# Optimization experiments

Hardware: AMD Instinct MI355X
Metric: run time of the kernel (lower is better)

Reference implementation:

```python
import jax, jax.numpy as jnp
import numpy as np

N_NODES = 100000
IN_DIM = 64
HID = 64
N_EDGES = 1600000
EPS = 1e-5
SLOPE = 0.01  # F.leaky_relu default


def _glorot(key, shape):
    fan_in, fan_out = shape[1], shape[0]
    lim = jnp.sqrt(6.0 / (fan_in + fan_out))
    return jax.random.uniform(key, shape, jnp.float32, -lim, lim)


def setup_inputs() -> dict:
    key = jax.random.key(0)
    ks = jax.random.split(key, 8)
    x = jax.random.normal(ks[0], (N_NODES, IN_DIM), jnp.float32)
    src = jax.random.randint(ks[1], (N_EDGES,), 0, N_NODES, jnp.int32)
    dst = jax.random.randint(ks[2], (N_EDGES,), 0, N_NODES, jnp.int32)
    edge_index = jnp.stack([src, dst])  # [2, E]
    return {
        "x": x,
        "edge_index": edge_index,
        "W_self1": _glorot(ks[3], (HID, IN_DIM)),
        "W_neigh1": _glorot(ks[4], (HID, IN_DIM)),
        "b1": jnp.zeros((HID,), jnp.float32),
        "gamma1": jnp.ones((HID,), jnp.float32),
        "beta1": jnp.zeros((HID,), jnp.float32),
        "W_self2": _glorot(ks[5], (HID, HID)),
        "W_neigh2": _glorot(ks[6], (HID, HID)),
        "b2": jnp.zeros((HID,), jnp.float32),
        "gamma2": jnp.ones((HID,), jnp.float32),
        "beta2": jnp.zeros((HID,), jnp.float32),
    }


def _sage_mean(h, src, dst, W_self, W_neigh, b):
    # neighbor mean aggregation: mean of src features at each dst node
    msg_sum = jax.ops.segment_sum(h[src], dst, num_segments=N_NODES)  # [N, d]
    deg = jax.ops.segment_sum(jnp.ones_like(dst, jnp.float32), dst, num_segments=N_NODES)
    h_neigh = msg_sum / jnp.maximum(deg, 1.0)[:, None]  # isolated nodes -> 0
    return h @ W_self.T + h_neigh @ W_neigh.T + b


def _bn(h, gamma, beta):
    mu = jnp.mean(h, axis=0)
    var = jnp.mean(jnp.square(h - mu), axis=0)
    return (h - mu) * jax.lax.rsqrt(var + EPS) * gamma + beta


def reference(x, edge_index, W_self1, W_neigh1, b1, gamma1, beta1,
              W_self2, W_neigh2, b2, gamma2, beta2):
    src, dst = edge_index[0], edge_index[1]
    h = _sage_mean(x, src, dst, W_self1, W_neigh1, b1)
    h = jax.nn.leaky_relu(_bn(h, gamma1, beta1), SLOPE)
    h = _sage_mean(h, src, dst, W_self2, W_neigh2, b2)
    h = jax.nn.leaky_relu(_bn(h, gamma2, beta2), SLOPE)
    return h
```

## Files before the change

kernel.cpp:

```cpp
#include <hip/hip_runtime.h>

#define EPS 1e-5f
#define SLOPE 0.01f

typedef short bf16x8 __attribute__((ext_vector_type(8)));
typedef float f32x4 __attribute__((ext_vector_type(4)));

static __device__ __forceinline__ unsigned short f2bf(float f) {
  unsigned u = __float_as_uint(f);
  unsigned r = (u + 0x7FFFu + ((u >> 16) & 1u)) >> 16;
  return (unsigned short)r;
}
#define BFLO(u) __uint_as_float((u) << 16)
#define BFHI(u) __uint_as_float((u) & 0xFFFF0000u)


__global__ __launch_bounds__(1024) void hist_cvt_kernel(
    const int* __restrict__ dst, int* __restrict__ hist, int E, int NB,
    int histBlocks, const float* __restrict__ x, unsigned short* __restrict__ xb,
    int total4) {
  extern __shared__ int lh[];
  if ((int)blockIdx.x < histBlocks) {
    for (int i = threadIdx.x; i < NB; i += blockDim.x) lh[i] = 0;
    __syncthreads();
    int stride = histBlocks * blockDim.x;
    for (int i = blockIdx.x * blockDim.x + threadIdx.x; i < E; i += stride)
      atomicAdd(&lh[((unsigned)dst[i]) >> 8], 1);
    __syncthreads();
    for (int b = threadIdx.x; b < NB; b += blockDim.x)
      hist[(size_t)b * histBlocks + blockIdx.x] = lh[b];
  } else {
    int cb = blockIdx.x - histBlocks;
    int stride = (gridDim.x - histBlocks) * blockDim.x;
    for (int i = cb * blockDim.x + threadIdx.x; i < total4; i += stride) {
      float4 v = reinterpret_cast<const float4*>(x)[i];
      ushort4 o;
      o.x = f2bf(v.x); o.y = f2bf(v.y); o.z = f2bf(v.z); o.w = f2bf(v.w);
      reinterpret_cast<ushort4*>(xb)[i] = o;
    }
  }
}

__global__ void scan_blk(const int* in, int* out, int* bsum, int n) {
  __shared__ int s[256];
  int i = blockIdx.x * 256 + threadIdx.x;
  int v = (i < n) ? in[i] : 0;
  s[threadIdx.x] = v;
  __syncthreads();
  for (int off = 1; off < 256; off <<= 1) {
    int t = (threadIdx.x >= off) ? s[threadIdx.x - off] : 0;
    __syncthreads();
    s[threadIdx.x] += t;
    __syncthreads();
  }
  if (i < n) out[i] = s[threadIdx.x] - v;
  if (threadIdx.x == 255) bsum[blockIdx.x] = s[255];
}

__global__ void scan_top(int* bsum, int nb) {
  __shared__ int s[512];
  int tid = threadIdx.x;
  int v = (tid < nb) ? bsum[tid] : 0;
  s[tid] = v;
  __syncthreads();
  for (int off = 1; off < 512; off <<= 1) {
    int t = (tid >= off) ? s[tid - off] : 0;
    __syncthreads();
    s[tid] += t;
    __syncthreads();
  }
  if (tid < nb) bsum[tid] = s[tid] - v;
}

__global__ void scan_add(int* out, const int* bsum, int n) {
  int i = blockIdx.x * 256 + threadIdx.x;
  if (i < n) out[i] += bsum[blockIdx.x];
}

__global__ __launch_bounds__(1024) void scatter_kernel(
    const int* __restrict__ src, const int* __restrict__ dst,
    const int* __restrict__ histS, unsigned* __restrict__ binned, int E, int NB) {
  extern __shared__ int cur[];
  for (int b = threadIdx.x; b < NB; b += blockDim.x)
    cur[b] = histS[(size_t)b * gridDim.x + blockIdx.x];
  __syncthreads();
  int stride = gridDim.x * blockDim.x;
  for (int i = blockIdx.x * blockDim.x + threadIdx.x; i < E; i += stride) {
    int d = dst[i];
    unsigned s = (unsigned)src[i];
    int b = ((unsigned)d) >> 8;
    int pos = atomicAdd(&cur[b], 1);
    binned[pos] = s | (((unsigned)d & 255u) << 20);
  }
}

__global__ __launch_bounds__(256) void fine_kernel(
    const unsigned* __restrict__ binned, const int* __restrict__ histS,
    int* __restrict__ rowptr, int* __restrict__ col, int E, int NB, int NBLKB, int N) {
  __shared__ int ldeg[256];
  __shared__ int lcur[256];
  __shared__ int ss[256];
  int b = blockIdx.x;
  int tid = threadIdx.x;
  int seg_s = histS[(size_t)b * NBLKB];
  int seg_e = (b + 1 < NB) ? histS[(size_t)(b + 1) * NBLKB] : E;
  ldeg[tid] = 0;
  __syncthreads();
  for (int i = seg_s + tid; i < seg_e; i += 256)
    atomicAdd(&ldeg[(binned[i] >> 20) & 255u], 1);
  __syncthreads();
  int d = ldeg[tid];
  ss[tid] = d;
  __syncthreads();
  for (int off = 1; off < 256; off <<= 1) {
    int t = (tid >= off) ? ss[tid - off] : 0;
    __syncthreads();
    ss[tid] += t;
    __syncthreads();
  }
  int base = seg_s + ss[tid] - d;
  lcur[tid] = base;
  int node = (b << 8) + tid;
  if (node < N) rowptr[node] = base;
  if (b == NB - 1 && tid == 0) rowptr[N] = E;
  __syncthreads();
  for (int i = seg_s + tid; i < seg_e; i += 256) {
    unsigned v = binned[i];
    int pos = atomicAdd(&lcur[(v >> 20) & 255u], 1);
    col[pos] = (int)(v & 0xFFFFFu);
  }
}


__global__ __launch_bounds__(256) void agg_kernel(
    const unsigned short* __restrict__ hb, const int* __restrict__ rowptr,
    const int* __restrict__ col, unsigned short* __restrict__ hm, int n) {
  int t = blockIdx.x * 256 + threadIdx.x;
  int node = t >> 3;
  int fo = (t & 7) * 8;
  if (node >= n) return;
  int beg = rowptr[node];
  int end = rowptr[node + 1];
  float s0 = 0.f, s1 = 0.f, s2 = 0.f, s3 = 0.f;
  float s4 = 0.f, s5 = 0.f, s6 = 0.f, s7 = 0.f;
  int e = beg;
  for (; e + 4 <= end; e += 4) {
    int i0 = col[e], i1 = col[e + 1], i2 = col[e + 2], i3 = col[e + 3];
    uint4 u0 = *reinterpret_cast<const uint4*>(&hb[(size_t)i0 * 64 + fo]);
    uint4 u1 = *reinterpret_cast<const uint4*>(&hb[(size_t)i1 * 64 + fo]);
    uint4 u2 = *reinterpret_cast<const uint4*>(&hb[(size_t)i2 * 64 + fo]);
    uint4 u3 = *reinterpret_cast<const uint4*>(&hb[(size_t)i3 * 64 + fo]);
    s0 += BFLO(u0.x) + BFLO(u1.x) + BFLO(u2.x) + BFLO(u3.x);
    s1 += BFHI(u0.x) + BFHI(u1.x) + BFHI(u2.x) + BFHI(u3.x);
    s2 += BFLO(u0.y) + BFLO(u1.y) + BFLO(u2.y) + BFLO(u3.y);
    s3 += BFHI(u0.y) + BFHI(u1.y) + BFHI(u2.y) + BFHI(u3.y);
    s4 += BFLO(u0.z) + BFLO(u1.z) + BFLO(u2.z) + BFLO(u3.z);
    s5 += BFHI(u0.z) + BFHI(u1.z) + BFHI(u2.z) + BFHI(u3.z);
    s6 += BFLO(u0.w) + BFLO(u1.w) + BFLO(u2.w) + BFLO(u3.w);
    s7 += BFHI(u0.w) + BFHI(u1.w) + BFHI(u2.w) + BFHI(u3.w);
  }
  for (; e < end; ++e) {
    uint4 u = *reinterpret_cast<const uint4*>(&hb[(size_t)col[e] * 64 + fo]);
    s0 += BFLO(u.x); s1 += BFHI(u.x);
    s2 += BFLO(u.y); s3 += BFHI(u.y);
    s4 += BFLO(u.z); s5 += BFHI(u.z);
    s6 += BFLO(u.w); s7 += BFHI(u.w);
  }
  int deg = end - beg;
  float inv = 1.0f / (float)(deg > 0 ? deg : 1);
  uint4 o;
  o.x = (unsigned)f2bf(s0 * inv) | ((unsigned)f2bf(s1 * inv) << 16);
  o.y = (unsigned)f2bf(s2 * inv) | ((unsigned)f2bf(s3 * inv) << 16);
  o.z = (unsigned)f2bf(s4 * inv) | ((unsigned)f2bf(s5 * inv) << 16);
  o.w = (unsigned)f2bf(s6 * inv) | ((unsigned)f2bf(s7 * inv) << 16);
  *reinterpret_cast<uint4*>(&hm[(size_t)node * 64 + fo]) = o;
}


__global__ __launch_bounds__(256) void gemm_stream(
    const unsigned short* __restrict__ A0,
    const unsigned short* __restrict__ A1,
    const float* __restrict__ Wself, const float* __restrict__ Wneigh,
    const float* __restrict__ bias,
    unsigned short* __restrict__ zb, float* __restrict__ partial, int n, int ntiles) {
  int tid = threadIdx.x;
  int lane = tid & 63;
  int w = tid >> 6;
  int l15 = lane & 15;
  int g = lane >> 4;

  bf16x8 B[4][4];
  #pragma unroll
  for (int t = 0; t < 4; ++t) {
    #pragma unroll
    for (int s = 0; s < 4; ++s) {
      const float* base = (s < 2 ? Wself : Wneigh) + (t * 16 + l15) * 64 + (s & 1) * 32 + g * 8;
      float4 w0 = *reinterpret_cast<const float4*>(base);
      float4 w1 = *reinterpret_cast<const float4*>(base + 4);
      bf16x8 b;
      b[0] = (short)f2bf(w0.x); b[1] = (short)f2bf(w0.y);
      b[2] = (short)f2bf(w0.z); b[3] = (short)f2bf(w0.w);
      b[4] = (short)f2bf(w1.x); b[5] = (short)f2bf(w1.y);
      b[6] = (short)f2bf(w1.z); b[7] = (short)f2bf(w1.w);
      B[t][s] = b;
    }
  }
  float bv[4];
  #pragma unroll
  for (int t = 0; t < 4; ++t) bv[t] = bias[t * 16 + l15];

  float ps[4] = {0.f, 0.f, 0.f, 0.f};
  float pq[4] = {0.f, 0.f, 0.f, 0.f};

  int nw = gridDim.x * 4;
  for (int tile = blockIdx.x * 4 + w; tile < ntiles; tile += nw) {
    int r0 = tile * 16 + l15;
    uint4 a[4];
    if (r0 < n) {
      const uint4* pa0 = reinterpret_cast<const uint4*>(A0 + (size_t)r0 * 64);
      const uint4* pa1 = reinterpret_cast<const uint4*>(A1 + (size_t)r0 * 64);
      a[0] = pa0[g]; a[1] = pa0[4 + g]; a[2] = pa1[g]; a[3] = pa1[4 + g];
    } else {
      a[0] = a[1] = a[2] = a[3] = make_uint4(0u, 0u, 0u, 0u);
    }
    f32x4 acc[4] = {};
    #pragma unroll
    for (int s = 0; s < 4; ++s) {
      bf16x8 af = *reinterpret_cast<bf16x8*>(&a[s]);
      #pragma unroll
      for (int t = 0; t < 4; ++t)
        acc[t] = __builtin_amdgcn_mfma_f32_16x16x32_bf16(af, B[t][s], acc[t], 0, 0, 0);
    }
    #pragma unroll
    for (int t = 0; t < 4; ++t) {
      #pragma unroll
      for (int i = 0; i < 4; ++i) {
        int gr = tile * 16 + g * 4 + i;
        if (gr < n) {
          float v = acc[t][i] + bv[t];
          zb[(size_t)gr * 64 + t * 16 + l15] = f2bf(v);
          ps[t] += v;
          pq[t] += v * v;
        }
      }
    }
  }

  #pragma unroll
  for (int t = 0; t < 4; ++t) {
    ps[t] += __shfl_xor(ps[t], 16); ps[t] += __shfl_xor(ps[t], 32);
    pq[t] += __shfl_xor(pq[t], 16); pq[t] += __shfl_xor(pq[t], 32);
  }
  __shared__ float sred[128];
  if (tid < 128) sred[tid] = 0.f;
  __syncthreads();
  if (lane < 16) {
    #pragma unroll
    for (int t = 0; t < 4; ++t) {
      atomicAdd(&sred[t * 16 + l15], ps[t]);
      atomicAdd(&sred[64 + t * 16 + l15], pq[t]);
    }
  }
  __syncthreads();
  if (tid < 128) partial[(size_t)blockIdx.x * 128 + tid] = sred[tid];
}

__global__ __launch_bounds__(256) void reduce_stats(const float* __restrict__ partial,
                                                    float* __restrict__ stats, int nblk) {
  int f = blockIdx.x;
  float s = 0.f;
  for (int j = threadIdx.x; j < nblk; j += 256) s += partial[(size_t)j * 128 + f];
  #pragma unroll
  for (int o = 1; o < 64; o <<= 1) s += __shfl_xor(s, o);
  __shared__ float r[4];
  if ((threadIdx.x & 63) == 0) r[threadIdx.x >> 6] = s;
  __syncthreads();
  if (threadIdx.x == 0) stats[f] = r[0] + r[1] + r[2] + r[3];
}


__global__ void bn_bf16_kernel(const unsigned short* __restrict__ zb,
                               const float* __restrict__ stats,
                               const float* __restrict__ gamma, const float* __restrict__ beta,
                               unsigned short* __restrict__ out, int n) {
  __shared__ float sc[64];
  __shared__ float sh[64];
  if (threadIdx.x < 64) {
    int f = threadIdx.x;
    float invN = 1.0f / (float)n;
    float mu = stats[f] * invN;
    float var = stats[64 + f] * invN - mu * mu;
    float s = rsqrtf(var + EPS) * gamma[f];
    sc[f] = s;
    sh[f] = beta[f] - mu * s;
  }
  __syncthreads();
  int total = n * 16;
  int stride = gridDim.x * blockDim.x;
  for (int idx = blockIdx.x * blockDim.x + threadIdx.x; idx < total; idx += stride) {
    int f0 = (idx & 15) * 4;
    uint2 u = reinterpret_cast<const uint2*>(zb)[idx];
    float t;
    ushort4 o;
    t = BFLO(u.x) * sc[f0 + 0] + sh[f0 + 0]; o.x = f2bf(t > 0.f ? t : SLOPE * t);
    t = BFHI(u.x) * sc[f0 + 1] + sh[f0 + 1]; o.y = f2bf(t > 0.f ? t : SLOPE * t);
    t = BFLO(u.y) * sc[f0 + 2] + sh[f0 + 2]; o.z = f2bf(t > 0.f ? t : SLOPE * t);
    t = BFHI(u.y) * sc[f0 + 3] + sh[f0 + 3]; o.w = f2bf(t > 0.f ? t : SLOPE * t);
    reinterpret_cast<ushort4*>(out)[idx] = o;
  }
}

__global__ void bn_f32_kernel(const unsigned short* __restrict__ zb,
                              const float* __restrict__ stats,
                              const float* __restrict__ gamma, const float* __restrict__ beta,
                              float* __restrict__ out, int n) {
  __shared__ float sc[64];
  __shared__ float sh[64];
  if (threadIdx.x < 64) {
    int f = threadIdx.x;
    float invN = 1.0f / (float)n;
    float mu = stats[f] * invN;
    float var = stats[64 + f] * invN - mu * mu;
    float s = rsqrtf(var + EPS) * gamma[f];
    sc[f] = s;
    sh[f] = beta[f] - mu * s;
  }
  __syncthreads();
  int total = n * 16;
  int stride = gridDim.x * blockDim.x;
  for (int idx = blockIdx.x * blockDim.x + threadIdx.x; idx < total; idx += stride) {
    int f0 = (idx & 15) * 4;
    uint2 u = reinterpret_cast<const uint2*>(zb)[idx];
    float4 o;
    float t;
    t = BFLO(u.x) * sc[f0 + 0] + sh[f0 + 0]; o.x = t > 0.f ? t : SLOPE * t;
    t = BFHI(u.x) * sc[f0 + 1] + sh[f0 + 1]; o.y = t > 0.f ? t : SLOPE * t;
    t = BFLO(u.y) * sc[f0 + 2] + sh[f0 + 2]; o.z = t > 0.f ? t : SLOPE * t;
    t = BFHI(u.y) * sc[f0 + 3] + sh[f0 + 3]; o.w = t > 0.f ? t : SLOPE * t;
    reinterpret_cast<float4*>(out)[idx] = o;
  }
}


extern "C" void kernel_launch(void* const* d_in, const int* in_sizes, int n_in,
                              void* d_out, int out_size, void* d_ws, size_t ws_size,
                              hipStream_t stream) {
  const float* x  = (const float*)d_in[0];
  const int* ei   = (const int*)d_in[1];
  const float* Ws1 = (const float*)d_in[2];
  const float* Wn1 = (const float*)d_in[3];
  const float* b1  = (const float*)d_in[4];
  const float* g1  = (const float*)d_in[5];
  const float* be1 = (const float*)d_in[6];
  const float* Ws2 = (const float*)d_in[7];
  const float* Wn2 = (const float*)d_in[8];
  const float* b2  = (const float*)d_in[9];
  const float* g2  = (const float*)d_in[10];
  const float* be2 = (const float*)d_in[11];
  float* out = (float*)d_out;

  int N = in_sizes[0] / 64;
  int E = in_sizes[1] / 2;
  const int* src = ei;
  const int* dst = ei + E;

  int NB = (N + 255) >> 8;
  const int NBLKB = 256;
  int M = NB * NBLKB;

  int ntiles = (N + 15) / 16;
  int gblk = (ntiles + 7) / 8;

  char* ws = (char*)d_ws;
  float* stats1 = (float*)ws;
  float* stats2 = stats1 + 128;
  size_t off = 1024;
  auto take = [&](size_t bytes) {
    void* p = ws + off;
    off = (off + bytes + 255) & ~(size_t)255;
    return p;
  };
  int* hist   = (int*)take((size_t)M * 4);
  int* bsum   = (int*)take(512 * 4);
  int* rowptr = (int*)take((size_t)(N + 1) * 4);
  unsigned* binned = (unsigned*)take((size_t)E * 4);
  int* col    = (int*)take((size_t)E * 4);
  unsigned short* xb  = (unsigned short*)take((size_t)N * 64 * 2);
  unsigned short* hmb = (unsigned short*)take((size_t)N * 64 * 2);
  unsigned short* h1b = (unsigned short*)take((size_t)N * 64 * 2);
  unsigned short* zb  = (unsigned short*)take((size_t)N * 64 * 2);
  float* partial = (float*)take((size_t)gblk * 128 * 4);

  hist_cvt_kernel<<<NBLKB + 128, 1024, NB * 4, stream>>>(dst, hist, E, NB, NBLKB,
                                                         x, xb, N * 16);
  int nb1 = (M + 255) / 256;
  scan_blk<<<nb1, 256, 0, stream>>>(hist, hist, bsum, M);
  scan_top<<<1, 512, 0, stream>>>(bsum, nb1);
  scan_add<<<nb1, 256, 0, stream>>>(hist, bsum, M);
  scatter_kernel<<<NBLKB, 1024, NB * 4, stream>>>(src, dst, hist, binned, E, NB);
  fine_kernel<<<NB, 256, 0, stream>>>(binned, hist, rowptr, col, E, NB, NBLKB, N);

  int ab = (N * 8 + 255) / 256;

  agg_kernel<<<ab, 256, 0, stream>>>(xb, rowptr, col, hmb, N);
  gemm_stream<<<gblk, 256, 0, stream>>>(xb, hmb, Ws1, Wn1, b1, zb, partial, N, ntiles);
  reduce_stats<<<128, 256, 0, stream>>>(partial, stats1, gblk);
  bn_bf16_kernel<<<2048, 256, 0, stream>>>(zb, stats1, g1, be1, h1b, N);

  agg_kernel<<<ab, 256, 0, stream>>>(h1b, rowptr, col, hmb, N);
  gemm_stream<<<gblk, 256, 0, stream>>>(h1b, hmb, Ws2, Wn2, b2, zb, partial, N, ntiles);
  reduce_stats<<<128, 256, 0, stream>>>(partial, stats2, gblk);
  bn_f32_kernel<<<2048, 256, 0, stream>>>(zb, stats2, g2, be2, out, N);
}
```

Before: 173.8 us.

## Fold scan_add into consumers, vectorize edge loads, unroll aggregation, precompute BN coefficients

Drops the scan_add launch by having scatter_kernel and fine_kernel add the per-bin block offsets themselves. Histogram and scatter now read dst/src as int4 vectors, with a scalar tail handled by block 0. The aggregation gather is unrolled to 8 neighbors per iteration to keep more loads in flight. The BN statistics reduction now computes scale and shift once per feature, so the BN kernels no longer recompute them in every block. Together these cut launch count and per-block overhead, at the cost of more registers in agg_kernel and extra gathers from bsum.

```diff
diff --git a/kernel.cpp b/kernel.cpp
--- a/kernel.cpp
+++ b/kernel.cpp
@@ -23,9 +23,20 @@
   if ((int)blockIdx.x < histBlocks) {
     for (int i = threadIdx.x; i < NB; i += blockDim.x) lh[i] = 0;
     __syncthreads();
+    int E4 = E >> 2;
     int stride = histBlocks * blockDim.x;
-    for (int i = blockIdx.x * blockDim.x + threadIdx.x; i < E; i += stride)
-      atomicAdd(&lh[((unsigned)dst[i]) >> 8], 1);
+    const int4* d4 = (const int4*)dst;
+    for (int i = blockIdx.x * blockDim.x + threadIdx.x; i < E4; i += stride) {
+      int4 d = d4[i];
+      atomicAdd(&lh[((unsigned)d.x) >> 8], 1);
+      atomicAdd(&lh[((unsigned)d.y) >> 8], 1);
+      atomicAdd(&lh[((unsigned)d.z) >> 8], 1);
+      atomicAdd(&lh[((unsigned)d.w) >> 8], 1);
+    }
+    if (blockIdx.x == 0) {
+      for (int i = (E4 << 2) + threadIdx.x; i < E; i += blockDim.x)
+        atomicAdd(&lh[((unsigned)dst[i]) >> 8], 1);
+    }
     __syncthreads();
     for (int b = threadIdx.x; b < NB; b += blockDim.x)
       hist[(size_t)b * histBlocks + blockIdx.x] = lh[b];
@@ -72,38 +83,50 @@
   if (tid < nb) bsum[tid] = s[tid] - v;
 }
 
-__global__ void scan_add(int* out, const int* bsum, int n) {
-  int i = blockIdx.x * 256 + threadIdx.x;
-  if (i < n) out[i] += bsum[blockIdx.x];
-}
-
 __global__ __launch_bounds__(1024) void scatter_kernel(
     const int* __restrict__ src, const int* __restrict__ dst,
-    const int* __restrict__ histS, unsigned* __restrict__ binned, int E, int NB) {
+    const int* __restrict__ histS, const int* __restrict__ bsum,
+    unsigned* __restrict__ binned, int E, int NB) {
   extern __shared__ int cur[];
   for (int b = threadIdx.x; b < NB; b += blockDim.x)
-    cur[b] = histS[(size_t)b * gridDim.x + blockIdx.x];
-  __syncthreads();
+    cur[b] = histS[(size_t)b * gridDim.x + blockIdx.x] + bsum[b];
+  __syncthreads();
+  int E4 = E >> 2;
   int stride = gridDim.x * blockDim.x;
-  for (int i = blockIdx.x * blockDim.x + threadIdx.x; i < E; i += stride) {
-    int d = dst[i];
-    unsigned s = (unsigned)src[i];
-    int b = ((unsigned)d) >> 8;
-    int pos = atomicAdd(&cur[b], 1);
-    binned[pos] = s | (((unsigned)d & 255u) << 20);
+  const int4* d4 = (const int4*)dst;
+  const int4* s4 = (const int4*)src;
+  for (int i = blockIdx.x * blockDim.x + threadIdx.x; i < E4; i += stride) {
+    int4 d = d4[i];
+    int4 s = s4[i];
+    int b0 = ((unsigned)d.x) >> 8;
+    binned[atomicAdd(&cur[b0], 1)] = (unsigned)s.x | (((unsigned)d.x & 255u) << 20);
+    int b1 = ((unsigned)d.y) >> 8;
+    binned[atomicAdd(&cur[b1], 1)] = (unsigned)s.y | (((unsigned)d.y & 255u) << 20);
+    int b2 = ((unsigned)d.z) >> 8;
+    binned[atomicAdd(&cur[b2], 1)] = (unsigned)s.z | (((unsigned)d.z & 255u) << 20);
+    int b3 = ((unsigned)d.w) >> 8;
+    binned[atomicAdd(&cur[b3], 1)] = (unsigned)s.w | (((unsigned)d.w & 255u) << 20);
+  }
+  if (blockIdx.x == 0) {
+    for (int i = (E4 << 2) + threadIdx.x; i < E; i += blockDim.x) {
+      int d = dst[i];
+      int b = ((unsigned)d) >> 8;
+      binned[atomicAdd(&cur[b], 1)] = (unsigned)src[i] | (((unsigned)d & 255u) << 20);
+    }
   }
 }
 
 __global__ __launch_bounds__(256) void fine_kernel(
     const unsigned* __restrict__ binned, const int* __restrict__ histS,
+    const int* __restrict__ bsum,
     int* __restrict__ rowptr, int* __restrict__ col, int E, int NB, int NBLKB, int N) {
   __shared__ int ldeg[256];
   __shared__ int lcur[256];
   __shared__ int ss[256];
   int b = blockIdx.x;
   int tid = threadIdx.x;
-  int seg_s = histS[(size_t)b * NBLKB];
-  int seg_e = (b + 1 < NB) ? histS[(size_t)(b + 1) * NBLKB] : E;
+  int seg_s = histS[(size_t)b * NBLKB] + bsum[b];
+  int seg_e = (b + 1 < NB) ? (histS[(size_t)(b + 1) * NBLKB] + bsum[b + 1]) : E;
   ldeg[tid] = 0;
   __syncthreads();
   for (int i = seg_s + tid; i < seg_e; i += 256)
@@ -144,20 +167,33 @@
   float s0 = 0.f, s1 = 0.f, s2 = 0.f, s3 = 0.f;
   float s4 = 0.f, s5 = 0.f, s6 = 0.f, s7 = 0.f;
   int e = beg;
-  for (; e + 4 <= end; e += 4) {
-    int i0 = col[e], i1 = col[e + 1], i2 = col[e + 2], i3 = col[e + 3];
+  for (; e + 8 <= end; e += 8) {
+    int i0 = col[e],     i1 = col[e + 1], i2 = col[e + 2], i3 = col[e + 3];
+    int i4 = col[e + 4], i5 = col[e + 5], i6 = col[e + 6], i7 = col[e + 7];
     uint4 u0 = *reinterpret_cast<const uint4*>(&hb[(size_t)i0 * 64 + fo]);
     uint4 u1 = *reinterpret_cast<const uint4*>(&hb[(size_t)i1 * 64 + fo]);
     uint4 u2 = *reinterpret_cast<const uint4*>(&hb[(size_t)i2 * 64 + fo]);
     uint4 u3 = *reinterpret_cast<const uint4*>(&hb[(size_t)i3 * 64 + fo]);
-    s0 += BFLO(u0.x) + BFLO(u1.x) + BFLO(u2.x) + BFLO(u3.x);
-    s1 += BFHI(u0.x) + BFHI(u1.x) + BFHI(u2.x) + BFHI(u3.x);
-    s2 += BFLO(u0.y) + BFLO(u1.y) + BFLO(u2.y) + BFLO(u3.y);
-    s3 += BFHI(u0.y) + BFHI(u1.y) + BFHI(u2.y) + BFHI(u3.y);
-    s4 += BFLO(u0.z) + BFLO(u1.z) + BFLO(u2.z) + BFLO(u3.z);
-    s5 += BFHI(u0.z) + BFHI(u1.z) + BFHI(u2.z) + BFHI(u3.z);
-    s6 += BFLO(u0.w) + BFLO(u1.w) + BFLO(u2.w) + BFLO(u3.w);
-    s7 += BFHI(u0.w) + BFHI(u1.w) + BFHI(u2.w) + BFHI(u3.w);
+    uint4 u4 = *reinterpret_cast<const uint4*>(&hb[(size_t)i4 * 64 + fo]);
+    uint4 u5 = *reinterpret_cast<const uint4*>(&hb[(size_t)i5 * 64 + fo]);
+    uint4 u6 = *reinterpret_cast<const uint4*>(&hb[(size_t)i6 * 64 + fo]);
+    uint4 u7 = *reinterpret_cast<const uint4*>(&hb[(size_t)i7 * 64 + fo]);
+    s0 += BFLO(u0.x) + BFLO(u1.x) + BFLO(u2.x) + BFLO(u3.x)
+        + BFLO(u4.x) + BFLO(u5.x) + BFLO(u6.x) + BFLO(u7.x);
+    s1 += BFHI(u0.x) + BFHI(u1.x) + BFHI(u2.x) + BFHI(u3.x)
+        + BFHI(u4.x) + BFHI(u5.x) + BFHI(u6.x) + BFHI(u7.x);
+    s2 += BFLO(u0.y) + BFLO(u1.y) + BFLO(u2.y) + BFLO(u3.y)
+        + BFLO(u4.y) + BFLO(u5.y) + BFLO(u6.y) + BFLO(u7.y);
+    s3 += BFHI(u0.y) + BFHI(u1.y) + BFHI(u2.y) + BFHI(u3.y)
+        + BFHI(u4.y) + BFHI(u5.y) + BFHI(u6.y) + BFHI(u7.y);
+    s4 += BFLO(u0.z) + BFLO(u1.z) + BFLO(u2.z) + BFLO(u3.z)
+        + BFLO(u4.z) + BFLO(u5.z) + BFLO(u6.z) + BFLO(u7.z);
+    s5 += BFHI(u0.z) + BFHI(u1.z) + BFHI(u2.z) + BFHI(u3.z)
+        + BFHI(u4.z) + BFHI(u5.z) + BFHI(u6.z) + BFHI(u7.z);
+    s6 += BFLO(u0.w) + BFLO(u1.w) + BFLO(u2.w) + BFLO(u3.w)
+        + BFLO(u4.w) + BFLO(u5.w) + BFLO(u6.w) + BFLO(u7.w);
+    s7 += BFHI(u0.w) + BFHI(u1.w) + BFHI(u2.w) + BFHI(u3.w)
+        + BFHI(u4.w) + BFHI(u5.w) + BFHI(u6.w) + BFHI(u7.w);
   }
   for (; e < end; ++e) {
     uint4 u = *reinterpret_cast<const uint4*>(&hb[(size_t)col[e] * 64 + fo]);
@@ -265,34 +301,46 @@
   if (tid < 128) partial[(size_t)blockIdx.x * 128 + tid] = sred[tid];
 }
 
-__global__ __launch_bounds__(256) void reduce_stats(const float* __restrict__ partial,
-                                                    float* __restrict__ stats, int nblk) {
+__global__ __launch_bounds__(256) void reduce_coef(
+    const float* __restrict__ partial, const float* __restrict__ gamma,
+    const float* __restrict__ beta, float* __restrict__ coef, int nblk, float invN) {
   int f = blockIdx.x;
-  float s = 0.f;
-  for (int j = threadIdx.x; j < nblk; j += 256) s += partial[(size_t)j * 128 + f];
+  float s = 0.f, q = 0.f;
+  for (int j = threadIdx.x; j < nblk; j += 256) {
+    s += partial[(size_t)j * 128 + f];
+    q += partial[(size_t)j * 128 + 64 + f];
+  }
   #pragma unroll
-  for (int o = 1; o < 64; o <<= 1) s += __shfl_xor(s, o);
-  __shared__ float r[4];
-  if ((threadIdx.x & 63) == 0) r[threadIdx.x >> 6] = s;
-  __syncthreads();
-  if (threadIdx.x == 0) stats[f] = r[0] + r[1] + r[2] + r[3];
+  for (int o = 1; o < 64; o <<= 1) {
+    s += __shfl_xor(s, o);
+    q += __shfl_xor(q, o);
+  }
+  __shared__ float rs[4], rq[4];
+  if ((threadIdx.x & 63) == 0) {
+    rs[threadIdx.x >> 6] = s;
+    rq[threadIdx.x >> 6] = q;
+  }
+  __syncthreads();
+  if (threadIdx.x == 0) {
+    float S = rs[0] + rs[1] + rs[2] + rs[3];
+    float Q = rq[0] + rq[1] + rq[2] + rq[3];
+    float mu = S * invN;
+    float var = Q * invN - mu * mu;
+    float sc = rsqrtf(var + EPS) * gamma[f];
+    coef[f] = sc;
+    coef[64 + f] = beta[f] - mu * sc;
+  }
 }
 
 
 __global__ void bn_bf16_kernel(const unsigned short* __restrict__ zb,
-                               const float* __restrict__ stats,
-                               const float* __restrict__ gamma, const float* __restrict__ beta,
+                               const float* __restrict__ coef,
                                unsigned short* __restrict__ out, int n) {
   __shared__ float sc[64];
   __shared__ float sh[64];
   if (threadIdx.x < 64) {
-    int f = threadIdx.x;
-    float invN = 1.0f / (float)n;
-    float mu = stats[f] * invN;
-    float var = stats[64 + f] * invN - mu * mu;
-    float s = rsqrtf(var + EPS) * gamma[f];
-    sc[f] = s;
-    sh[f] = beta[f] - mu * s;
+    sc[threadIdx.x] = coef[threadIdx.x];
+    sh[threadIdx.x] = coef[64 + threadIdx.x];
   }
   __syncthreads();
   int total = n * 16;
@@ -311,19 +359,13 @@
 }
 
 __global__ void bn_f32_kernel(const unsigned short* __restrict__ zb,
-                              const float* __restrict__ stats,
-                              const float* __restrict__ gamma, const float* __restrict__ beta,
+                              const float* __restrict__ coef,
                               float* __restrict__ out, int n) {
   __shared__ float sc[64];
   __shared__ float sh[64];
   if (threadIdx.x < 64) {
-    int f = threadIdx.x;
-    float invN = 1.0f / (float)n;
-    float mu = stats[f] * invN;
-    float var = stats[64 + f] * invN - mu * mu;
-    float s = rsqrtf(var + EPS) * gamma[f];
-    sc[f] = s;
-    sh[f] = beta[f] - mu * s;
+    sc[threadIdx.x] = coef[threadIdx.x];
+    sh[threadIdx.x] = coef[64 + threadIdx.x];
   }
   __syncthreads();
   int total = n * 16;
@@ -372,8 +414,8 @@
   int gblk = (ntiles + 7) / 8;
 
   char* ws = (char*)d_ws;
-  float* stats1 = (float*)ws;
-  float* stats2 = stats1 + 128;
+  float* coef1 = (float*)ws;
+  float* coef2 = coef1 + 128;
   size_t off = 1024;
   auto take = [&](size_t bytes) {
     void* p = ws + off;
@@ -396,19 +438,19 @@
   int nb1 = (M + 255) / 256;
   scan_blk<<<nb1, 256, 0, stream>>>(hist, hist, bsum, M);
   scan_top<<<1, 512, 0, stream>>>(bsum, nb1);
-  scan_add<<<nb1, 256, 0, stream>>>(hist, bsum, M);
-  scatter_kernel<<<NBLKB, 1024, NB * 4, stream>>>(src, dst, hist, binned, E, NB);
-  fine_kernel<<<NB, 256, 0, stream>>>(binned, hist, rowptr, col, E, NB, NBLKB, N);
+  scatter_kernel<<<NBLKB, 1024, NB * 4, stream>>>(src, dst, hist, bsum, binned, E, NB);
+  fine_kernel<<<NB, 256, 0, stream>>>(binned, hist, bsum, rowptr, col, E, NB, NBLKB, N);
 
   int ab = (N * 8 + 255) / 256;
+  float invN = 1.0f / (float)N;
 
   agg_kernel<<<ab, 256, 0, stream>>>(xb, rowptr, col, hmb, N);
   gemm_stream<<<gblk, 256, 0, stream>>>(xb, hmb, Ws1, Wn1, b1, zb, partial, N, ntiles);
-  reduce_stats<<<128, 256, 0, stream>>>(partial, stats1, gblk);
-  bn_bf16_kernel<<<2048, 256, 0, stream>>>(zb, stats1, g1, be1, h1b, N);
+  reduce_coef<<<64, 256, 0, stream>>>(partial, g1, be1, coef1, gblk, invN);
+  bn_bf16_kernel<<<2048, 256, 0, stream>>>(zb, coef1, h1b, N);
 
   agg_kernel<<<ab, 256, 0, stream>>>(h1b, rowptr, col, hmb, N);
   gemm_stream<<<gblk, 256, 0, stream>>>(h1b, hmb, Ws2, Wn2, b2, zb, partial, N, ntiles);
-  reduce_stats<<<128, 256, 0, stream>>>(partial, stats2, gblk);
-  bn_f32_kernel<<<2048, 256, 0, stream>>>(zb, stats2, g2, be2, out, N);
-}
+  reduce_coef<<<64, 256, 0, stream>>>(partial, g2, be2, coef2, gblk, invN);
+  bn_f32_kernel<<<2048, 256, 0, stream>>>(zb, coef2, out, N);
+}
```

Measured after the change: 184.2 us. 6.0% more time.
